# Kernel tuning notes

Hardware: AMD Instinct MI355X
Metric: run time of the kernel (lower is better)

The kernel has to match this reference:

```python
import jax, jax.numpy as jnp
import numpy as np

N = 50000          # total particles (nodes)
E = 800000         # num edges
D = 256            # embed_dim
H = 8              # num_heads
ED = 6             # edge_dim
HD = D // H // 2   # head_dim = 16
LAMBDA_INIT = 1.0 - float(np.exp(-1.0))  # lambda_init_fn(depth=1)


def setup_inputs() -> dict:
    key = jax.random.key(0)
    ks = jax.random.split(key, 9)
    sc = lambda k, shape, fan_in: jax.random.normal(k, shape, jnp.float32) * (fan_in ** -0.5)
    x = jax.random.normal(ks[0], (N, D), jnp.float32)
    edge_index = jax.random.randint(ks[1], (2, E), 0, N, dtype=jnp.int64)
    edge_attr = jax.random.normal(ks[2], (E, ED), jnp.float32)
    v_w = sc(ks[3], (D, D), D)
    out_w = sc(ks[4], (D, D), D)
    e_w1 = sc(ks[5], (D, ED), ED)
    e_b1 = jnp.zeros((D,), jnp.float32)
    e_w2 = sc(ks[6], (2 * H, D), D)
    e_b2 = jnp.zeros((2 * H,), jnp.float32)
    lambda_q1 = 0.1 * jax.random.normal(ks[7], (100,), jnp.float32)
    lambda_k1 = 0.1 * jax.random.normal(ks[8], (100,), jnp.float32)
    return {"x": x, "edge_attr": edge_attr, "v_w": v_w, "out_w": out_w,
            "e_w1": e_w1, "e_b1": e_b1, "e_w2": e_w2, "e_b2": e_b2,
            "lambda_q1": lambda_q1, "lambda_k1": lambda_k1,
            "edge_index": edge_index}


def _scatter_softmax(scores, tgt, n):
    # numerically-stable segment softmax over edges grouped by tgt node
    m = jax.ops.segment_max(scores, tgt, num_segments=n)      # [n, H]
    e = jnp.exp(scores - m[tgt])                              # [E, H]
    s = jax.ops.segment_sum(e, tgt, num_segments=n)           # [n, H]
    return e / s[tgt]


def reference(x, edge_attr, v_w, out_w, e_w1, e_b1, e_w2, e_b2,
              lambda_q1, lambda_k1, edge_index):
    src, tgt = edge_index[0], edge_index[1]
    # V projection (no bias), split into heads of size 2*head_dim
    V = (x @ v_w.T).reshape(N, H, 2 * HD)
    # edge encoder MLP: Linear -> GELU(exact) -> Linear
    h = jax.nn.gelu(edge_attr @ e_w1.T + e_b1, approximate=False)
    edge_scores = (h @ e_w2.T + e_b2).reshape(E, H, 2)
    a1 = _scatter_softmax(edge_scores[:, :, 0], tgt, N)
    a2 = _scatter_softmax(edge_scores[:, :, 1], tgt, N)
    lambda_1 = jnp.exp(jnp.sum(lambda_q1 * lambda_k1))
    beta = jax.nn.sigmoid(lambda_1 * LAMBDA_INIT)
    attn_weights = a1 - beta * a2                              # [E, H]
    weighted_V = attn_weights[:, :, None] * V[src]             # [E, H, 2*HD]
    out = jax.ops.segment_sum(weighted_V, tgt, num_segments=N).reshape(N, D)
    out = out @ out_w.T
    return out, attn_weights, beta
```

## Files before the change

### kernel.cpp

```cpp
#include <hip/hip_runtime.h>
#include <hip/hip_bf16.h>
#include <math.h>

#define N_NODES 50000
#define N_EDGES 800000
#define DIM 256
#define HEADS 8
#define LAMBDA_INIT 0.63212055882855767f

using bf16x8 = __attribute__((ext_vector_type(8))) short;
using bf16x4 = __attribute__((ext_vector_type(4))) short;
using f32x4  = __attribute__((ext_vector_type(4))) float;
using f32x2  = __attribute__((ext_vector_type(2))) float;
#define MFMA16(a, b, c) __builtin_amdgcn_mfma_f32_16x16x32_bf16(a, b, c, 0, 0, 0)

__device__ __forceinline__ short f2b(float f) {
    __hip_bfloat16 h = __float2bfloat16(f);
    return *reinterpret_cast<short*>(&h);
}
__device__ __forceinline__ float b2f(short s) {
    unsigned u = ((unsigned)(unsigned short)s) << 16;
    return __uint_as_float(u);
}
__device__ __forceinline__ unsigned cvt_pk_bf16(float a, float b) {
    unsigned r;
    asm("v_cvt_pk_bf16_f32 %0, %1, %2" : "=v"(r) : "v"(a), "v"(b));
    return r;
}

__device__ __forceinline__ float gelu_f(float x) {
    float az = 0.70710678118654752f * fabsf(x);
    float t  = __builtin_amdgcn_rcpf(fmaf(0.47047f, az, 1.f));
    float q  = fmaf(fmaf(0.3739278f, t, -0.0479399f), t, 0.1740121f) * t;
    float E  = __expf(-az * az);
    return fmaf(-q * E, fabsf(x), fmaxf(x, 0.f));
}

__global__ __launch_bounds__(256) void scan1(const int* __restrict__ cnt,
                                             int* __restrict__ offs,
                                             int* __restrict__ partials, int n) {
    __shared__ int sh[256];
    int i = blockIdx.x * 256 + threadIdx.x;
    int v = (i < n) ? cnt[i] : 0;
    sh[threadIdx.x] = v;
    __syncthreads();
    for (int s = 1; s < 256; s <<= 1) {
        int add = (threadIdx.x >= s) ? sh[threadIdx.x - s] : 0;
        __syncthreads();
        sh[threadIdx.x] += add;
        __syncthreads();
    }
    if (i < n) offs[i] = sh[threadIdx.x] - v;
    if (threadIdx.x == 255) partials[blockIdx.x] = sh[255];
}

__global__ __launch_bounds__(256) void scan2(int* __restrict__ partials, int nb,
                                             const float* __restrict__ lq,
                                             const float* __restrict__ lk,
                                             float* __restrict__ beta_ws,
                                             float* __restrict__ beta_out) {
    __shared__ int sh[256];
    __shared__ float redb[128];
    int tid = threadIdx.x;
    int v = (tid < nb) ? partials[tid] : 0;
    sh[tid] = v;
    __syncthreads();
    for (int s = 1; s < 256; s <<= 1) {
        int add = (tid >= s) ? sh[tid - s] : 0;
        __syncthreads();
        sh[tid] += add;
        __syncthreads();
    }
    if (tid < nb) partials[tid] = sh[tid] - v;

    if (tid < 128) {
        float b = 0.f;
        for (int i = tid; i < 100; i += 128) b += lq[i] * lk[i];
        redb[tid] = b;
    }
    __syncthreads();
    for (int s = 64; s > 0; s >>= 1) {
        if (tid < s) redb[tid] += redb[tid + s];
        __syncthreads();
    }
    if (tid == 0) {
        float l1 = expf(redb[0]);
        float b = 1.f / (1.f + expf(-l1 * LAMBDA_INIT));
        *beta_ws = b;
        *beta_out = b;
    }
}

__global__ __launch_bounds__(256) void scan3(int* __restrict__ offs,
                                             const int* __restrict__ partials,
                                             int* __restrict__ cursor, int n) {
    int i = blockIdx.x * 256 + threadIdx.x;
    if (i < n) {
        int o = offs[i] + partials[blockIdx.x];
        offs[i] = o;
        cursor[i] = o;
    }
    if (i == 0) offs[n] = N_EDGES;
}

template <bool ABF, bool CBF>
__global__ __launch_bounds__(256) void gemm_mfma_t(const void* __restrict__ Av,
                                                   const float* __restrict__ W,
                                                   void* __restrict__ Cv, int M,
                                                   const int* __restrict__ hist_tgt,
                                                   int* __restrict__ hist_cnt) {
    __shared__ __align__(16) short As[128 * 40];
    __shared__ __align__(16) short Ws[64 * 40];
    int tid = threadIdx.x;
    int lane = tid & 63, wv = tid >> 6;
    int l16 = lane & 15, quad = lane >> 4;
    int bm = blockIdx.x * 128, bn = blockIdx.y * 64;

    if (hist_tgt) {
        int gtid = (blockIdx.x * 4 + blockIdx.y) * 256 + tid;
        int e0 = gtid * 2;
        if (e0 < N_EDGES)     atomicAdd(&hist_cnt[hist_tgt[e0]], 1);
        if (e0 + 1 < N_EDGES) atomicAdd(&hist_cnt[hist_tgt[e0 + 1]], 1);
    }

    f32x4 acc[2][4];
#pragma unroll
    for (int mt = 0; mt < 2; ++mt)
#pragma unroll
        for (int nt = 0; nt < 4; ++nt) acc[mt][nt] = (f32x4){0.f, 0.f, 0.f, 0.f};

    int r = tid >> 1, hf = tid & 1;
    int rw = (tid & 127) >> 1, hw = tid & 1;

    for (int k0 = 0; k0 < 256; k0 += 32) {
        {
            int m = bm + r;
            bf16x8 p0, p1;
            if (ABF) {
                if (m < M) {
                    const bf16x8* ap =
                        (const bf16x8*)&((const short*)Av)[(size_t)m * 256 + k0 + hf * 16];
                    p0 = ap[0]; p1 = ap[1];
                } else {
                    p0 = (bf16x8){0,0,0,0,0,0,0,0}; p1 = p0;
                }
            } else {
                float4 f0, f1, f2, f3;
                if (m < M) {
                    const float4* ap =
                        (const float4*)&((const float*)Av)[(size_t)m * 256 + k0 + hf * 16];
                    f0 = ap[0]; f1 = ap[1]; f2 = ap[2]; f3 = ap[3];
                } else {
                    f0 = f1 = f2 = f3 = make_float4(0.f, 0.f, 0.f, 0.f);
                }
                p0[0]=f2b(f0.x); p0[1]=f2b(f0.y); p0[2]=f2b(f0.z); p0[3]=f2b(f0.w);
                p0[4]=f2b(f1.x); p0[5]=f2b(f1.y); p0[6]=f2b(f1.z); p0[7]=f2b(f1.w);
                p1[0]=f2b(f2.x); p1[1]=f2b(f2.y); p1[2]=f2b(f2.z); p1[3]=f2b(f2.w);
                p1[4]=f2b(f3.x); p1[5]=f2b(f3.y); p1[6]=f2b(f3.z); p1[7]=f2b(f3.w);
            }
            *(bf16x8*)&As[r * 40 + hf * 16]     = p0;
            *(bf16x8*)&As[r * 40 + hf * 16 + 8] = p1;
        }
        if (tid < 128) {
            const float4* wp = (const float4*)&W[(size_t)(bn + rw) * 256 + k0 + hw * 16];
            float4 f0 = wp[0], f1 = wp[1], f2 = wp[2], f3 = wp[3];
            bf16x8 p0, p1;
            p0[0]=f2b(f0.x); p0[1]=f2b(f0.y); p0[2]=f2b(f0.z); p0[3]=f2b(f0.w);
            p0[4]=f2b(f1.x); p0[5]=f2b(f1.y); p0[6]=f2b(f1.z); p0[7]=f2b(f1.w);
            p1[0]=f2b(f2.x); p1[1]=f2b(f2.y); p1[2]=f2b(f2.z); p1[3]=f2b(f2.w);
            p1[4]=f2b(f3.x); p1[5]=f2b(f3.y); p1[6]=f2b(f3.z); p1[7]=f2b(f3.w);
            *(bf16x8*)&Ws[rw * 40 + hw * 16]     = p0;
            *(bf16x8*)&Ws[rw * 40 + hw * 16 + 8] = p1;
        }
        __syncthreads();
#pragma unroll
        for (int mt = 0; mt < 2; ++mt) {
            bf16x8 afr = *(bf16x8*)&As[(wv * 32 + mt * 16 + l16) * 40 + quad * 8];
#pragma unroll
            for (int nt = 0; nt < 4; ++nt) {
                bf16x8 bfr = *(bf16x8*)&Ws[(nt * 16 + l16) * 40 + quad * 8];
                acc[mt][nt] = MFMA16(afr, bfr, acc[mt][nt]);
            }
        }
        __syncthreads();
    }
#pragma unroll
    for (int mt = 0; mt < 2; ++mt) {
#pragma unroll
        for (int rr = 0; rr < 4; ++rr) {
            int m = bm + wv * 32 + mt * 16 + quad * 4 + rr;
            if (m < M) {
#pragma unroll
                for (int nt = 0; nt < 4; ++nt) {
                    if (CBF)
                        ((short*)Cv)[(size_t)m * 256 + bn + nt * 16 + l16] =
                            f2b(acc[mt][nt][rr]);
                    else
                        ((float*)Cv)[(size_t)m * 256 + bn + nt * 16 + l16] =
                            acc[mt][nt][rr];
                }
            }
        }
    }
}

__global__ __launch_bounds__(256) void edge_mlp_mfma(const float* __restrict__ edge_attr,
                                                     const float* __restrict__ e_w1,
                                                     const float* __restrict__ e_b1,
                                                     const float* __restrict__ e_w2,
                                                     const float* __restrict__ e_b2,
                                                     const int* __restrict__ tgt,
                                                     const int* __restrict__ srcp,
                                                     int* __restrict__ cursor,
                                                     float* __restrict__ sorted_sc,
                                                     int* __restrict__ slot_eid,
                                                     int* __restrict__ slot_src) {
    __shared__ __align__(16) short w1s[256 * 8];
    __shared__ __align__(16) float b1s[256];
    __shared__ __align__(16) float ea_s[256 * 6];
    __shared__ int slot_lds[4][64];

    int tid = threadIdx.x;
    int lane = tid & 63, wv = tid >> 6;
    int l16 = lane & 15, quad = lane >> 4;
    long eblk = (long)blockIdx.x * 256 + wv * 64;

    {
        int e = (int)(eblk + lane);
        int p = atomicAdd(&cursor[tgt[e]], 1);
        slot_lds[wv][lane] = p;
        slot_eid[p] = e;
        slot_src[p] = srcp[e];
    }

    {
        int n = tid;
#pragma unroll
        for (int k = 0; k < 6; ++k) w1s[n * 8 + k] = f2b(e_w1[n * 6 + k]);
        w1s[n * 8 + 6] = 0; w1s[n * 8 + 7] = 0;
        b1s[n] = e_b1[n];
    }
    {
        size_t base = (size_t)blockIdx.x * (256 * 6);
#pragma unroll
        for (int it = 0; it < 6; ++it) {
            int i = tid + it * 256;
            ea_s[i] = edge_attr[base + i];
        }
    }

    bf16x8 w2f[8];
#pragma unroll
    for (int c = 0; c < 8; ++c) {
#pragma unroll
        for (int j = 0; j < 8; ++j) {
            int col = c * 32 + ((j & 4) ? 16 : 0) + quad * 4 + (j & 3);
            w2f[c][j] = f2b(e_w2[l16 * 256 + col]);
        }
    }
    float b2r = e_b2[l16];
    __syncthreads();

    bf16x8 bfr[4];
#pragma unroll
    for (int g = 0; g < 4; ++g) {
        bfr[g] = (bf16x8){0, 0, 0, 0, 0, 0, 0, 0};
        if (quad == 0) {
            const float* p = &ea_s[(wv * 64 + g * 16 + l16) * 6];
#pragma unroll
            for (int j = 0; j < 6; ++j) bfr[g][j] = f2b(p[j]);
        }
    }

    f32x4 acc[4];
#pragma unroll
    for (int g = 0; g < 4; ++g) acc[g] = (f32x4){0.f, 0.f, 0.f, 0.f};

#pragma unroll
    for (int c2 = 0; c2 < 8; ++c2) {
        bf16x8 af0 = (bf16x8){0, 0, 0, 0, 0, 0, 0, 0};
        bf16x8 af1 = (bf16x8){0, 0, 0, 0, 0, 0, 0, 0};
        if (quad == 0) {
            af0 = *(bf16x8*)&w1s[((2 * c2) * 16 + l16) * 8];
            af1 = *(bf16x8*)&w1s[((2 * c2 + 1) * 16 + l16) * 8];
        }
        f32x4 bb0 = *(const f32x4*)&b1s[(2 * c2) * 16 + quad * 4];
        f32x4 bb1 = *(const f32x4*)&b1s[(2 * c2 + 1) * 16 + quad * 4];
#pragma unroll
        for (int g = 0; g < 4; ++g) {
            f32x4 cc0 = MFMA16(af0, bfr[g], bb0);
            f32x4 cc1 = MFMA16(af1, bfr[g], bb1);
            unsigned pw[4];
            pw[0] = cvt_pk_bf16(gelu_f(cc0[0]), gelu_f(cc0[1]));
            pw[1] = cvt_pk_bf16(gelu_f(cc0[2]), gelu_f(cc0[3]));
            pw[2] = cvt_pk_bf16(gelu_f(cc1[0]), gelu_f(cc1[1]));
            pw[3] = cvt_pk_bf16(gelu_f(cc1[2]), gelu_f(cc1[3]));
            bf16x8 pa = *reinterpret_cast<bf16x8*>(pw);
            acc[g] = MFMA16(pa, w2f[c2], acc[g]);
        }
    }

#pragma unroll
    for (int g = 0; g < 4; ++g) {
#pragma unroll
        for (int rr = 0; rr < 4; ++rr) {
            int p = slot_lds[wv][g * 16 + quad * 4 + rr];
            sorted_sc[(size_t)p * 16 + l16] = acc[g][rr] + b2r;
        }
    }
}

__global__ __launch_bounds__(256) void node_agg4(const int* __restrict__ slot_eid,
                                                 const int* __restrict__ offs,
                                                 const int* __restrict__ slot_src,
                                                 const float* __restrict__ sorted_sc,
                                                 const short* __restrict__ Vb,
                                                 const float* __restrict__ betap,
                                                 short* __restrict__ accumb,
                                                 float* __restrict__ attn_out) {
    __shared__ __align__(16) float scr_all[4][16 * 65];
    __shared__ __align__(16) float ms_all[4][32];
    __shared__ int src_all[4][64];

    int tid = threadIdx.x;
    int wv = tid >> 6, lane = tid & 63;
    int n = blockIdx.x * 4 + wv;
    float* scr = scr_all[wv];
    float* ms  = ms_all[wv];
    int* srcs  = src_all[wv];

    int beg = offs[n];
    int deg = offs[n + 1] - beg;
    int c16 = lane & 15, q4 = lane >> 4;
    int d0 = lane * 4, hh = lane >> 3;

    if (deg == 0) {
        bf16x4 z = (bf16x4){0, 0, 0, 0};
        *(bf16x4*)&accumb[(size_t)n * 256 + d0] = z;
        return;
    }
    float beta = *betap;

    if (deg <= 64) {
        int k = lane;
        int eid = 0, src = 0;
        float sc[16];
        if (k < deg) {
            int slot = beg + k;
            eid = slot_eid[slot];
            src = slot_src[slot];
            const f32x4* sp = (const f32x4*)&sorted_sc[(size_t)slot * 16];
            f32x4 s0 = sp[0], s1 = sp[1], s2 = sp[2], s3 = sp[3];
            sc[0]=s0[0]; sc[1]=s0[1]; sc[2]=s0[2]; sc[3]=s0[3];
            sc[4]=s1[0]; sc[5]=s1[1]; sc[6]=s1[2]; sc[7]=s1[3];
            sc[8]=s2[0]; sc[9]=s2[1]; sc[10]=s2[2]; sc[11]=s2[3];
            sc[12]=s3[0]; sc[13]=s3[1]; sc[14]=s3[2]; sc[15]=s3[3];
        } else {
#pragma unroll
            for (int c = 0; c < 16; ++c) sc[c] = -INFINITY;
        }
        srcs[k] = src;
#pragma unroll
        for (int c = 0; c < 16; ++c) scr[c * 65 + k] = sc[c];

        float mloc = -INFINITY;
        for (int j = 0; 4 * j < deg; ++j)
            mloc = fmaxf(mloc, scr[c16 * 65 + 4 * j + q4]);
        mloc = fmaxf(mloc, __shfl_xor(mloc, 16));
        mloc = fmaxf(mloc, __shfl_xor(mloc, 32));
        float sloc = 0.f;
        for (int j = 0; 4 * j < deg; ++j)
            sloc += __expf(scr[c16 * 65 + 4 * j + q4] - mloc);
        sloc += __shfl_xor(sloc, 16);
        sloc += __shfl_xor(sloc, 32);
        if (lane < 16) {
            ms[c16] = mloc;
            ms[16 + c16] = __builtin_amdgcn_rcpf(sloc);
        }

        if (k < deg) {
            float w[8];
#pragma unroll
            for (int h = 0; h < 8; ++h) {
                f32x2 mp = *(const f32x2*)&ms[2 * h];
                f32x2 rp = *(const f32x2*)&ms[16 + 2 * h];
                w[h] = __expf(sc[2 * h] - mp[0]) * rp[0]
                     - beta * __expf(sc[2 * h + 1] - mp[1]) * rp[1];
            }
            f32x4 w0 = (f32x4){w[0], w[1], w[2], w[3]};
            f32x4 w1 = (f32x4){w[4], w[5], w[6], w[7]};
            *(f32x4*)&attn_out[(size_t)eid * 8]     = w0;
            *(f32x4*)&attn_out[(size_t)eid * 8 + 4] = w1;
            *(f32x4*)&scr[k * 8]     = w0;
            *(f32x4*)&scr[k * 8 + 4] = w1;
        }

        float a0 = 0.f, a1 = 0.f, a2 = 0.f, a3 = 0.f;
        for (int kk = 0; kk < deg; ++kk) {
            float wk = scr[kk * 8 + hh];
            int sk = srcs[kk];
            bf16x4 v = *(const bf16x4*)&Vb[(size_t)sk * 256 + d0];
            a0 += wk * b2f(v[0]);
            a1 += wk * b2f(v[1]);
            a2 += wk * b2f(v[2]);
            a3 += wk * b2f(v[3]);
        }
        bf16x4 r;
        r[0] = f2b(a0); r[1] = f2b(a1); r[2] = f2b(a2); r[3] = f2b(a3);
        *(bf16x4*)&accumb[(size_t)n * 256 + d0] = r;
        return;
    }

    float m_run = -INFINITY, s_run = 0.f;
    for (int base = 0; base < deg; base += 64) {
        int k = base + lane;
        float sc[16];
        if (k < deg) {
            const f32x4* sp = (const f32x4*)&sorted_sc[(size_t)(beg + k) * 16];
            f32x4 s0 = sp[0], s1 = sp[1], s2 = sp[2], s3 = sp[3];
            sc[0]=s0[0]; sc[1]=s0[1]; sc[2]=s0[2]; sc[3]=s0[3];
            sc[4]=s1[0]; sc[5]=s1[1]; sc[6]=s1[2]; sc[7]=s1[3];
            sc[8]=s2[0]; sc[9]=s2[1]; sc[10]=s2[2]; sc[11]=s2[3];
            sc[12]=s3[0]; sc[13]=s3[1]; sc[14]=s3[2]; sc[15]=s3[3];
        } else {
#pragma unroll
            for (int c = 0; c < 16; ++c) sc[c] = -INFINITY;
        }
#pragma unroll
        for (int c = 0; c < 16; ++c) scr[c * 65 + lane] = sc[c];
        float mc = -INFINITY;
#pragma unroll
        for (int j = 0; j < 16; ++j)
            mc = fmaxf(mc, scr[c16 * 65 + 4 * j + q4]);
        mc = fmaxf(mc, __shfl_xor(mc, 16));
        mc = fmaxf(mc, __shfl_xor(mc, 32));
        float m_new = fmaxf(m_run, mc);
        float ssum = 0.f;
#pragma unroll
        for (int j = 0; j < 16; ++j)
            ssum += __expf(scr[c16 * 65 + 4 * j + q4] - m_new);
        ssum += __shfl_xor(ssum, 16);
        ssum += __shfl_xor(ssum, 32);
        s_run = s_run * __expf(m_run - m_new) + ssum;
        m_run = m_new;
    }
    if (lane < 16) {
        ms[c16] = m_run;
        ms[16 + c16] = __builtin_amdgcn_rcpf(s_run);
    }

    float a0 = 0.f, a1 = 0.f, a2 = 0.f, a3 = 0.f;
    for (int base = 0; base < deg; base += 64) {
        int k = base + lane;
        int cn = min(64, deg - base);
        int src = 0;
        if (lane < cn) {
            int slot = beg + k;
            int eid = slot_eid[slot];
            src = slot_src[slot];
            const f32x4* sp = (const f32x4*)&sorted_sc[(size_t)slot * 16];
            f32x4 s0 = sp[0], s1 = sp[1], s2 = sp[2], s3 = sp[3];
            float sc[16];
            sc[0]=s0[0]; sc[1]=s0[1]; sc[2]=s0[2]; sc[3]=s0[3];
            sc[4]=s1[0]; sc[5]=s1[1]; sc[6]=s1[2]; sc[7]=s1[3];
            sc[8]=s2[0]; sc[9]=s2[1]; sc[10]=s2[2]; sc[11]=s2[3];
            sc[12]=s3[0]; sc[13]=s3[1]; sc[14]=s3[2]; sc[15]=s3[3];
            float w[8];
#pragma unroll
            for (int h = 0; h < 8; ++h) {
                f32x2 mp = *(const f32x2*)&ms[2 * h];
                f32x2 rp = *(const f32x2*)&ms[16 + 2 * h];
                w[h] = __expf(sc[2 * h] - mp[0]) * rp[0]
                     - beta * __expf(sc[2 * h + 1] - mp[1]) * rp[1];
            }
            f32x4 w0 = (f32x4){w[0], w[1], w[2], w[3]};
            f32x4 w1 = (f32x4){w[4], w[5], w[6], w[7]};
            *(f32x4*)&attn_out[(size_t)eid * 8]     = w0;
            *(f32x4*)&attn_out[(size_t)eid * 8 + 4] = w1;
            *(f32x4*)&scr[lane * 8]     = w0;
            *(f32x4*)&scr[lane * 8 + 4] = w1;
        }
        srcs[lane] = src;
        for (int kk = 0; kk < cn; ++kk) {
            float wk = scr[kk * 8 + hh];
            int sk = srcs[kk];
            bf16x4 v = *(const bf16x4*)&Vb[(size_t)sk * 256 + d0];
            a0 += wk * b2f(v[0]);
            a1 += wk * b2f(v[1]);
            a2 += wk * b2f(v[2]);
            a3 += wk * b2f(v[3]);
        }
    }
    bf16x4 r;
    r[0] = f2b(a0); r[1] = f2b(a1); r[2] = f2b(a2); r[3] = f2b(a3);
    *(bf16x4*)&accumb[(size_t)n * 256 + d0] = r;
}

extern "C" void kernel_launch(void* const* d_in, const int* in_sizes, int n_in,
                              void* d_out, int out_size, void* d_ws, size_t ws_size,
                              hipStream_t stream) {
    const float* x         = (const float*)d_in[0];
    const float* edge_attr = (const float*)d_in[1];
    const float* v_w       = (const float*)d_in[2];
    const float* out_w     = (const float*)d_in[3];
    const float* e_w1      = (const float*)d_in[4];
    const float* e_b1      = (const float*)d_in[5];
    const float* e_w2      = (const float*)d_in[6];
    const float* e_b2      = (const float*)d_in[7];
    const float* lq        = (const float*)d_in[8];
    const float* lk        = (const float*)d_in[9];
    const int*   ei        = (const int*)d_in[10];
    const int* srcp = ei;
    const int* tgtp = ei + N_EDGES;

    float* out = (float*)d_out;
    float* attn_out = out + (size_t)N_NODES * 256;
    float* beta_out = attn_out + (size_t)N_EDGES * 8;

    short* Vb       = (short*)d_ws;
    float* sorted_sc= (float*)(Vb + (size_t)N_NODES * 256);
    short* accumb   = (short*)(sorted_sc + (size_t)N_EDGES * 16);
    int*   cnt      = (int*)(accumb + (size_t)N_NODES * 256);
    int*   offs     = cnt + N_NODES;
    int*   cursor   = offs + N_NODES + 1;
    int*   partials = cursor + N_NODES;
    int*   slot_eid = partials + 256;
    int*   slot_src = slot_eid + N_EDGES;
    float* betap    = (float*)(slot_src + N_EDGES);

    const int NB = (N_NODES + 255) / 256;

    hipMemsetAsync(cnt, 0, N_NODES * sizeof(int), stream);

    gemm_mfma_t<false, true><<<dim3((N_NODES + 127) / 128, 4), 256, 0, stream>>>(
        x, v_w, Vb, N_NODES, tgtp, cnt);

    scan1<<<NB, 256, 0, stream>>>(cnt, offs, partials, N_NODES);
    scan2<<<1, 256, 0, stream>>>(partials, NB, lq, lk, betap, beta_out);
    scan3<<<NB, 256, 0, stream>>>(offs, partials, cursor, N_NODES);

    edge_mlp_mfma<<<N_EDGES / 256, 256, 0, stream>>>(edge_attr, e_w1, e_b1, e_w2, e_b2,
                                                     tgtp, srcp, cursor,
                                                     sorted_sc, slot_eid, slot_src);

    node_agg4<<<N_NODES / 4, 256, 0, stream>>>(slot_eid, offs, slot_src, sorted_sc,
                                               Vb, betap, accumb, attn_out);

    gemm_mfma_t<true, false><<<dim3((N_NODES + 127) / 128, 4), 256, 0, stream>>>(
        accumb, out_w, out, N_NODES, nullptr, nullptr);
}
```

Baseline: 421.0 us.

## Pre-cast x to bf16 and enlarge GEMM tiles to 128x128

Adds a cast kernel that converts x to bf16 once (reusing the accumb buffer) and zeroes the histogram counts, replacing the memset. Both GEMMs now use a 128x128 block tile with a 2x2 wave layout and 4x4 MFMA tiles per wave, halving the column-block count. The goal is to stop re-reading and re-converting fp32 x across four column blocks and to raise operand reuse per LDS load. The cost is an extra kernel launch, an extra pass over x, and higher register pressure from the larger accumulator array.

Result: no change. 423.2 us (+0.5%).

```diff
diff --git a/kernel.cpp b/kernel.cpp
--- a/kernel.cpp
+++ b/kernel.cpp
@@ -34,6 +34,21 @@
     float q  = fmaf(fmaf(0.3739278f, t, -0.0479399f), t, 0.1740121f) * t;
     float E  = __expf(-az * az);
     return fmaf(-q * E, fabsf(x), fmaxf(x, 0.f));
+}
+
+__global__ __launch_bounds__(256) void cast_x(const float* __restrict__ x,
+                                              short* __restrict__ xb,
+                                              int* __restrict__ cnt) {
+    int gid = blockIdx.x * 256 + threadIdx.x;
+    if (gid < N_NODES) cnt[gid] = 0;
+    const int total = N_NODES * 256 / 8;
+    for (int p = gid; p < total; p += gridDim.x * 256) {
+        const float4* src = (const float4*)&x[(size_t)p * 8];
+        float4 a = src[0], b = src[1];
+        unsigned pw[4] = {cvt_pk_bf16(a.x, a.y), cvt_pk_bf16(a.z, a.w),
+                          cvt_pk_bf16(b.x, b.y), cvt_pk_bf16(b.z, b.w)};
+        *(bf16x8*)&xb[(size_t)p * 8] = *reinterpret_cast<bf16x8*>(pw);
+    }
 }
 
 __global__ __launch_bounds__(256) void scan1(const int* __restrict__ cnt,
@@ -103,101 +118,88 @@
     if (i == 0) offs[n] = N_EDGES;
 }
 
-template <bool ABF, bool CBF>
-__global__ __launch_bounds__(256) void gemm_mfma_t(const void* __restrict__ Av,
-                                                   const float* __restrict__ W,
-                                                   void* __restrict__ Cv, int M,
-                                                   const int* __restrict__ hist_tgt,
-                                                   int* __restrict__ hist_cnt) {
+template <bool CBF>
+__global__ __launch_bounds__(256) void gemm_bf16(const short* __restrict__ A,
+                                                 const float* __restrict__ W,
+                                                 void* __restrict__ Cv, int M,
+                                                 const int* __restrict__ hist_tgt,
+                                                 int* __restrict__ hist_cnt) {
     __shared__ __align__(16) short As[128 * 40];
-    __shared__ __align__(16) short Ws[64 * 40];
+    __shared__ __align__(16) short Ws[128 * 40];
     int tid = threadIdx.x;
     int lane = tid & 63, wv = tid >> 6;
     int l16 = lane & 15, quad = lane >> 4;
-    int bm = blockIdx.x * 128, bn = blockIdx.y * 64;
+    int bm = blockIdx.x * 128, bn = blockIdx.y * 128;
+    int wr = wv >> 1, wc = wv & 1;
 
     if (hist_tgt) {
-        int gtid = (blockIdx.x * 4 + blockIdx.y) * 256 + tid;
-        int e0 = gtid * 2;
-        if (e0 < N_EDGES)     atomicAdd(&hist_cnt[hist_tgt[e0]], 1);
-        if (e0 + 1 < N_EDGES) atomicAdd(&hist_cnt[hist_tgt[e0 + 1]], 1);
-    }
-
-    f32x4 acc[2][4];
-#pragma unroll
-    for (int mt = 0; mt < 2; ++mt)
+        int gtid = (blockIdx.x * 2 + blockIdx.y) * 256 + tid;
+#pragma unroll
+        for (int u = 0; u < 4; ++u) {
+            int e = gtid * 4 + u;
+            if (e < N_EDGES) atomicAdd(&hist_cnt[hist_tgt[e]], 1);
+        }
+    }
+
+    f32x4 acc[4][4];
+#pragma unroll
+    for (int mt = 0; mt < 4; ++mt)
 #pragma unroll
         for (int nt = 0; nt < 4; ++nt) acc[mt][nt] = (f32x4){0.f, 0.f, 0.f, 0.f};
 
     int r = tid >> 1, hf = tid & 1;
-    int rw = (tid & 127) >> 1, hw = tid & 1;
 
     for (int k0 = 0; k0 < 256; k0 += 32) {
         {
             int m = bm + r;
             bf16x8 p0, p1;
-            if (ABF) {
-                if (m < M) {
-                    const bf16x8* ap =
-                        (const bf16x8*)&((const short*)Av)[(size_t)m * 256 + k0 + hf * 16];
-                    p0 = ap[0]; p1 = ap[1];
-                } else {
-                    p0 = (bf16x8){0,0,0,0,0,0,0,0}; p1 = p0;
-                }
+            if (m < M) {
+                const bf16x8* ap = (const bf16x8*)&A[(size_t)m * 256 + k0 + hf * 16];
+                p0 = ap[0]; p1 = ap[1];
             } else {
-                float4 f0, f1, f2, f3;
-                if (m < M) {
-                    const float4* ap =
-                        (const float4*)&((const float*)Av)[(size_t)m * 256 + k0 + hf * 16];
-                    f0 = ap[0]; f1 = ap[1]; f2 = ap[2]; f3 = ap[3];
-                } else {
-                    f0 = f1 = f2 = f3 = make_float4(0.f, 0.f, 0.f, 0.f);
-                }
-                p0[0]=f2b(f0.x); p0[1]=f2b(f0.y); p0[2]=f2b(f0.z); p0[3]=f2b(f0.w);
-                p0[4]=f2b(f1.x); p0[5]=f2b(f1.y); p0[6]=f2b(f1.z); p0[7]=f2b(f1.w);
-                p1[0]=f2b(f2.x); p1[1]=f2b(f2.y); p1[2]=f2b(f2.z); p1[3]=f2b(f2.w);
-                p1[4]=f2b(f3.x); p1[5]=f2b(f3.y); p1[6]=f2b(f3.z); p1[7]=f2b(f3.w);
+                p0 = (bf16x8){0,0,0,0,0,0,0,0}; p1 = p0;
             }
             *(bf16x8*)&As[r * 40 + hf * 16]     = p0;
             *(bf16x8*)&As[r * 40 + hf * 16 + 8] = p1;
         }
-        if (tid < 128) {
-            const float4* wp = (const float4*)&W[(size_t)(bn + rw) * 256 + k0 + hw * 16];
+        {
+            const float4* wp = (const float4*)&W[(size_t)(bn + r) * 256 + k0 + hf * 16];
             float4 f0 = wp[0], f1 = wp[1], f2 = wp[2], f3 = wp[3];
-            bf16x8 p0, p1;
-            p0[0]=f2b(f0.x); p0[1]=f2b(f0.y); p0[2]=f2b(f0.z); p0[3]=f2b(f0.w);
-            p0[4]=f2b(f1.x); p0[5]=f2b(f1.y); p0[6]=f2b(f1.z); p0[7]=f2b(f1.w);
-            p1[0]=f2b(f2.x); p1[1]=f2b(f2.y); p1[2]=f2b(f2.z); p1[3]=f2b(f2.w);
-            p1[4]=f2b(f3.x); p1[5]=f2b(f3.y); p1[6]=f2b(f3.z); p1[7]=f2b(f3.w);
-            *(bf16x8*)&Ws[rw * 40 + hw * 16]     = p0;
-            *(bf16x8*)&Ws[rw * 40 + hw * 16 + 8] = p1;
-        }
-        __syncthreads();
-#pragma unroll
-        for (int mt = 0; mt < 2; ++mt) {
-            bf16x8 afr = *(bf16x8*)&As[(wv * 32 + mt * 16 + l16) * 40 + quad * 8];
-#pragma unroll
-            for (int nt = 0; nt < 4; ++nt) {
-                bf16x8 bfr = *(bf16x8*)&Ws[(nt * 16 + l16) * 40 + quad * 8];
-                acc[mt][nt] = MFMA16(afr, bfr, acc[mt][nt]);
-            }
-        }
-        __syncthreads();
-    }
-#pragma unroll
-    for (int mt = 0; mt < 2; ++mt) {
+            unsigned pw[8];
+            pw[0] = cvt_pk_bf16(f0.x, f0.y); pw[1] = cvt_pk_bf16(f0.z, f0.w);
+            pw[2] = cvt_pk_bf16(f1.x, f1.y); pw[3] = cvt_pk_bf16(f1.z, f1.w);
+            pw[4] = cvt_pk_bf16(f2.x, f2.y); pw[5] = cvt_pk_bf16(f2.z, f2.w);
+            pw[6] = cvt_pk_bf16(f3.x, f3.y); pw[7] = cvt_pk_bf16(f3.z, f3.w);
+            *(bf16x8*)&Ws[r * 40 + hf * 16]     = *reinterpret_cast<bf16x8*>(&pw[0]);
+            *(bf16x8*)&Ws[r * 40 + hf * 16 + 8] = *reinterpret_cast<bf16x8*>(&pw[4]);
+        }
+        __syncthreads();
+        bf16x8 bq[4];
+#pragma unroll
+        for (int nt = 0; nt < 4; ++nt)
+            bq[nt] = *(bf16x8*)&Ws[(wc * 64 + nt * 16 + l16) * 40 + quad * 8];
+#pragma unroll
+        for (int mt = 0; mt < 4; ++mt) {
+            bf16x8 afr = *(bf16x8*)&As[(wr * 64 + mt * 16 + l16) * 40 + quad * 8];
+#pragma unroll
+            for (int nt = 0; nt < 4; ++nt)
+                acc[mt][nt] = MFMA16(afr, bq[nt], acc[mt][nt]);
+        }
+        __syncthreads();
+    }
+#pragma unroll
+    for (int mt = 0; mt < 4; ++mt) {
 #pragma unroll
         for (int rr = 0; rr < 4; ++rr) {
-            int m = bm + wv * 32 + mt * 16 + quad * 4 + rr;
+            int m = bm + wr * 64 + mt * 16 + quad * 4 + rr;
             if (m < M) {
 #pragma unroll
                 for (int nt = 0; nt < 4; ++nt) {
+                    int col = bn + wc * 64 + nt * 16 + l16;
                     if (CBF)
-                        ((short*)Cv)[(size_t)m * 256 + bn + nt * 16 + l16] =
-                            f2b(acc[mt][nt][rr]);
+                        ((short*)Cv)[(size_t)m * 256 + col] = f2b(acc[mt][nt][rr]);
                     else
-                        ((float*)Cv)[(size_t)m * 256 + bn + nt * 16 + l16] =
-                            acc[mt][nt][rr];
+                        ((float*)Cv)[(size_t)m * 256 + col] = acc[mt][nt][rr];
                 }
             }
         }
@@ -528,12 +530,14 @@
     int*   slot_src = slot_eid + N_EDGES;
     float* betap    = (float*)(slot_src + N_EDGES);
 
+    short* xb = accumb;
+
     const int NB = (N_NODES + 255) / 256;
 
-    hipMemsetAsync(cnt, 0, N_NODES * sizeof(int), stream);
-
-    gemm_mfma_t<false, true><<<dim3((N_NODES + 127) / 128, 4), 256, 0, stream>>>(
-        x, v_w, Vb, N_NODES, tgtp, cnt);
+    cast_x<<<2048, 256, 0, stream>>>(x, xb, cnt);
+
+    gemm_bf16<true><<<dim3((N_NODES + 127) / 128, 2), 256, 0, stream>>>(
+        xb, v_w, Vb, N_NODES, tgtp, cnt);
 
     scan1<<<NB, 256, 0, stream>>>(cnt, offs, partials, N_NODES);
     scan2<<<1, 256, 0, stream>>>(partials, NB, lq, lk, betap, beta_out);
@@ -546,6 +550,6 @@
     node_agg4<<<N_NODES / 4, 256, 0, stream>>>(slot_eid, offs, slot_src, sorted_sc,
                                                Vb, betap, accumb, attn_out);
 
-    gemm_mfma_t<true, false><<<dim3((N_NODES + 127) / 128, 4), 256, 0, stream>>>(
+    gemm_bf16<false><<<dim3((N_NODES + 127) / 128, 2), 256, 0, stream>>>(
         accumb, out_w, out, N_NODES, nullptr, nullptr);
 }
```
